# Kernel optimization log

Hardware: AMD Instinct MI355X
Metric: run time of the kernel (lower is better)

The kernel has to match this reference:

```python
import jax, jax.numpy as jnp
import numpy as np

DROPOUT_P = 0.1  # module-level constant in the source
DROP_KEY = jax.random.key(42)

B, H, S, D = 4, 16, 1024, 64


def setup_inputs() -> dict:
    key = jax.random.key(0)
    kq, kk, kv = jax.random.split(key, 3)
    return {
        "query": jax.random.normal(kq, (B, H, S, D), dtype=jnp.float32),
        "key": jax.random.normal(kk, (B, H, S, D), dtype=jnp.float32),
        "value": jax.random.normal(kv, (B, H, S, D), dtype=jnp.float32),
        "scale_factor": 8,
    }


def reference(query, key, value, scale_factor):
    # qk = query @ key^T                         [B,H,S,S]
    qk = jnp.einsum("bhqd,bhkd->bhqk", query, key)
    # source divides by inv_scale = 1/scale_factor -> multiply by scale_factor
    scaled_qk = qk * jnp.float32(scale_factor)
    softmax_qk = jax.nn.softmax(scaled_qk, axis=-1)
    # inverted dropout with fixed key (deterministic reference)
    keep = jax.random.bernoulli(DROP_KEY, 1.0 - DROPOUT_P, softmax_qk.shape)
    dropout_qk = jnp.where(keep, softmax_qk / (1.0 - DROPOUT_P), 0.0)
    # output = attn @ value                      [B,H,S,D]
    return jnp.einsum("bhqk,bhkd->bhqd", dropout_qk, value)
```

## Files before the change

### kernel.cpp

```cpp
#include <hip/hip_runtime.h>
#include <stdint.h>
#include <math.h>


constexpr int Bn = 4, Hn = 16, Sn = 1024, Dn = 64;
constexpr int NT = 256;
constexpr int TQ = 128, TK = 64;
constexpr int PST = 72;
constexpr int CAP = 512;

typedef short s16x8 __attribute__((ext_vector_type(8)));
typedef float f32x4 __attribute__((ext_vector_type(4)));

__device__ __forceinline__ uint16_t f2bf(float x) {
  uint32_t u = __float_as_uint(x);
  return (uint16_t)((u + 0x7fffu + ((u >> 16) & 1u)) >> 16);
}
__device__ __forceinline__ float bf2f(uint16_t h) {
  return __uint_as_float(((uint32_t)h) << 16);
}

__device__ __forceinline__ void tf_round(uint32_t& x0, uint32_t& x1, const int r) {
  x0 += x1;
  x1 = (x1 << r) | (x1 >> (32 - r));
  x1 ^= x0;
}

__device__ __noinline__ int keep_bit(uint32_t j) {
  uint32_t x0 = 0u, x1 = j;
  const uint32_t k0 = 0u, k1v = 42u;
  const uint32_t k2v = k0 ^ k1v ^ 0x1BD11BDAu;
  x0 += k0; x1 += k1v;
  tf_round(x0, x1, 13); tf_round(x0, x1, 15); tf_round(x0, x1, 26); tf_round(x0, x1, 6);
  x0 += k1v; x1 += k2v + 1u;
  tf_round(x0, x1, 17); tf_round(x0, x1, 29); tf_round(x0, x1, 16); tf_round(x0, x1, 24);
  x0 += k2v; x1 += k0 + 2u;
  tf_round(x0, x1, 13); tf_round(x0, x1, 15); tf_round(x0, x1, 26); tf_round(x0, x1, 6);
  x0 += k0; x1 += k1v + 3u;
  tf_round(x0, x1, 17); tf_round(x0, x1, 29); tf_round(x0, x1, 16); tf_round(x0, x1, 24);
  x0 += k1v; x1 += k2v + 4u;
  tf_round(x0, x1, 13); tf_round(x0, x1, 15); tf_round(x0, x1, 26); tf_round(x0, x1, 6);
  x0 += k2v; x1 += k0 + 5u;
  uint32_t bits = x0 ^ x1;
  float u = __uint_as_float((bits >> 9) | 0x3f800000u) - 1.0f;
  return u < 0.9f;
}

__global__ __launch_bounds__(NT) void prep_kv(const float* __restrict__ K,
                                              const float* __restrict__ V,
                                              uint16_t* __restrict__ Khg,
                                              uint16_t* __restrict__ Klg,
                                              uint16_t* __restrict__ Vtg) {
  __shared__ float Vl[TK][Dn + 1];
  const int t = threadIdx.x;
  const int kt = blockIdx.x;
  const int bh = blockIdx.y;
  const int r = t >> 2, qd = t & 3;
  const size_t tile = ((size_t)bh * 16 + kt) * 4096;
  const float* ksrc = K + ((size_t)bh * Sn + (size_t)(kt * TK + r)) * Dn + qd * 16;
  const float* vsrc = V + ((size_t)bh * Sn + (size_t)(kt * TK + r)) * Dn + qd * 16;

#pragma unroll
  for (int half = 0; half < 2; ++half) {
    float4 a = *(const float4*)(ksrc + half * 8);
    float4 b = *(const float4*)(ksrc + half * 8 + 4);
    float xs[8] = {a.x, a.y, a.z, a.w, b.x, b.y, b.z, b.w};
    s16x8 hv, lv;
#pragma unroll
    for (int j = 0; j < 8; ++j) {
      uint16_t hb = f2bf(xs[j]);
      hv[j] = (short)hb;
      lv[j] = (short)f2bf(xs[j] - bf2f(hb));
    }
    const int sc = (qd * 2 + half) ^ (r & 7);
    *(s16x8*)&Khg[tile + (size_t)r * 64 + sc * 8] = hv;
    *(s16x8*)&Klg[tile + (size_t)r * 64 + sc * 8] = lv;
    float4 va = *(const float4*)(vsrc + half * 8);
    float4 vb = *(const float4*)(vsrc + half * 8 + 4);
    *(float4*)&Vl[r][qd * 16 + half * 8] = va;
    *(float4*)&Vl[r][qd * 16 + half * 8 + 4] = vb;
  }
  __syncthreads();
#pragma unroll
  for (int half = 0; half < 2; ++half) {
    s16x8 ov;
#pragma unroll
    for (int j = 0; j < 8; ++j) ov[j] = (short)f2bf(Vl[qd * 16 + half * 8 + j][r]);
    const int sc = (qd * 2 + half) ^ (r & 7);
    *(s16x8*)&Vtg[tile + (size_t)r * 64 + sc * 8] = ov;
  }
}

__global__ __launch_bounds__(NT) void attn_mfma3(
    const float* __restrict__ Q, const uint16_t* __restrict__ Khg,
    const uint16_t* __restrict__ Klg, const uint16_t* __restrict__ Vtg,
    const float* __restrict__ V, const int* __restrict__ scale_ptr,
    float* __restrict__ out) {
  __shared__ uint16_t KhS[TK * Dn];
  __shared__ uint16_t KlS[TK * Dn];
  __shared__ uint16_t VtS[Dn * TK];
  __shared__ uint16_t PS[4 * 32 * PST];
  __shared__ uint32_t Lm[4][CAP];
  __shared__ float Lsv[4][CAP];
  __shared__ float mfin[4][32];

  const int t = threadIdx.x;
  const int w = t >> 6;
  const int lane = t & 63;
  const int l16 = lane & 15;
  const int quad = lane >> 4;

  const int b = blockIdx.z, h = blockIdx.y;
  const int qbase = blockIdx.x * TQ;
  const int bh = b * Hn + h;
  const float qscale = (float)(*scale_ptr);

  s16x8 qh[2][2], ql[2][2];
#pragma unroll
  for (int u = 0; u < 2; ++u) {
    const int qrow = qbase + u * 64 + w * 16 + l16;
    const float* src = Q + ((size_t)bh * Sn + (size_t)qrow) * Dn;
#pragma unroll
    for (int ks = 0; ks < 2; ++ks) {
      float4 x0 = *(const float4*)(src + ks * 32 + quad * 8);
      float4 x1 = *(const float4*)(src + ks * 32 + quad * 8 + 4);
      float xv[8] = {x0.x, x0.y, x0.z, x0.w, x1.x, x1.y, x1.z, x1.w};
#pragma unroll
      for (int j = 0; j < 8; ++j) {
        const float xs = xv[j] * qscale;
        uint16_t hb = f2bf(xs);
        qh[u][ks][j] = (short)hb;
        ql[u][ks][j] = (short)f2bf(xs - bf2f(hb));
      }
    }
  }

  float m_r[2][4], l_r[2][4];
#pragma unroll
  for (int u = 0; u < 2; ++u)
#pragma unroll
    for (int r = 0; r < 4; ++r) { m_r[u][r] = -INFINITY; l_r[u][r] = 0.0f; }
  f32x4 o_acc[2][4];
#pragma unroll
  for (int u = 0; u < 2; ++u)
#pragma unroll
    for (int c = 0; c < 4; ++c) o_acc[u][c] = (f32x4){0.f, 0.f, 0.f, 0.f};

  const uint32_t hbase = (uint32_t)bh * (uint32_t)Sn;
  int lbase = 0;

  for (int kt = 0; kt < Sn / TK; ++kt) {
    const int kbase = kt * TK;
    __syncthreads();

    {
      const size_t tile = ((size_t)bh * 16 + kt) * 4096;
#pragma unroll
      for (int s = 0; s < 2; ++s) {
        const int eoff = (w * 2 + s) * 512 + lane * 8;
        __builtin_amdgcn_global_load_lds(
            (const __attribute__((address_space(1))) uint32_t*)(Khg + tile + eoff),
            (__attribute__((address_space(3))) uint32_t*)(KhS + eoff), 16, 0, 0);
        __builtin_amdgcn_global_load_lds(
            (const __attribute__((address_space(1))) uint32_t*)(Klg + tile + eoff),
            (__attribute__((address_space(3))) uint32_t*)(KlS + eoff), 16, 0, 0);
        __builtin_amdgcn_global_load_lds(
            (const __attribute__((address_space(1))) uint32_t*)(Vtg + tile + eoff),
            (__attribute__((address_space(3))) uint32_t*)(VtS + eoff), 16, 0, 0);
      }
    }
    __syncthreads();

    f32x4 sacc[2][4];
#pragma unroll
    for (int u = 0; u < 2; ++u)
#pragma unroll
      for (int c = 0; c < 4; ++c) sacc[u][c] = (f32x4){0.f, 0.f, 0.f, 0.f};
#pragma unroll
    for (int ks = 0; ks < 2; ++ks) {
#pragma unroll
      for (int c = 0; c < 4; ++c) {
        const int boff = (c * 16 + l16) * 64 + (((ks * 4 + quad) ^ (l16 & 7)) * 8);
        const s16x8 bhv = *(const s16x8*)&KhS[boff];
        const s16x8 blv = *(const s16x8*)&KlS[boff];
#pragma unroll
        for (int u = 0; u < 2; ++u) {
          sacc[u][c] = __builtin_amdgcn_mfma_f32_16x16x32_bf16(qh[u][ks], bhv, sacc[u][c], 0, 0, 0);
          sacc[u][c] = __builtin_amdgcn_mfma_f32_16x16x32_bf16(ql[u][ks], bhv, sacc[u][c], 0, 0, 0);
          sacc[u][c] = __builtin_amdgcn_mfma_f32_16x16x32_bf16(qh[u][ks], blv, sacc[u][c], 0, 0, 0);
        }
      }
    }

#pragma unroll
    for (int u = 0; u < 2; ++u) {
      float mx[4], al[4];
#pragma unroll
      for (int r = 0; r < 4; ++r) {
        mx[r] = fmaxf(fmaxf(sacc[u][0][r], sacc[u][1][r]),
                      fmaxf(sacc[u][2][r], sacc[u][3][r]));
#pragma unroll
        for (int d = 1; d < 16; d <<= 1) mx[r] = fmaxf(mx[r], __shfl_xor(mx[r], d));
        const float mn = fmaxf(m_r[u][r], mx[r]);
        al[r] = __expf(m_r[u][r] - mn);
        m_r[u][r] = mn;
      }
#pragma unroll
      for (int c = 0; c < 4; ++c)
#pragma unroll
        for (int r = 0; r < 4; ++r) o_acc[u][c][r] *= al[r];

      float rs[4] = {0.f, 0.f, 0.f, 0.f};
#pragma unroll
      for (int r = 0; r < 4; ++r) {
        float dv[4], pv[4];
#pragma unroll
        for (int c = 0; c < 4; ++c) {
          dv[c] = sacc[u][c][r] - m_r[u][r];
          pv[c] = __expf(dv[c]);
          rs[r] += pv[c];
        }
        const float dmx = fmaxf(fmaxf(dv[0], dv[1]), fmaxf(dv[2], dv[3]));
        if (__ballot(dmx > -11.0f) != 0ull) {
#pragma unroll
          for (int c = 0; c < 4; ++c) {
            const uint64_t mc = __ballot(dv[c] > -11.0f);
            if (mc != 0ull) {
              if (lbase + 64 <= CAP) {
                const int slot = lbase + (int)__popcll(mc & ((1ull << lane) - 1ull));
                if (dv[c] > -11.0f) {
                  const uint32_t rw = (uint32_t)(u * 16 + quad * 4 + r);
                  Lm[w][slot] = (rw << 10) | (uint32_t)(kbase + c * 16 + l16);
                  Lsv[w][slot] = dv[c] + m_r[u][r];
                }
                lbase += (int)__popcll(mc);
              } else if (dv[c] > -11.0f) {
                const uint32_t j =
                    (hbase + (uint32_t)(qbase + u * 64 + w * 16 + quad * 4 + r)) *
                        (uint32_t)Sn +
                    (uint32_t)(kbase + c * 16 + l16);
                if (!keep_bit(j)) pv[c] = 0.0f;
              }
            }
          }
        }
        const int prow = (w * 32 + u * 16 + quad * 4 + r) * PST;
#pragma unroll
        for (int c = 0; c < 4; ++c) PS[prow + c * 16 + l16] = f2bf(pv[c]);
      }
#pragma unroll
      for (int r = 0; r < 4; ++r) {
#pragma unroll
        for (int d = 1; d < 16; d <<= 1) rs[r] += __shfl_xor(rs[r], d);
        l_r[u][r] = l_r[u][r] * al[r] + rs[r];
      }
    }

#pragma unroll
    for (int ks2 = 0; ks2 < 2; ++ks2) {
      s16x8 pa[2];
#pragma unroll
      for (int u = 0; u < 2; ++u)
        pa[u] = *(const s16x8*)&PS[(w * 32 + u * 16 + l16) * PST + ks2 * 32 + quad * 8];
#pragma unroll
      for (int c = 0; c < 4; ++c) {
        const int voff = (c * 16 + l16) * 64 + (((ks2 * 4 + quad) ^ (l16 & 7)) * 8);
        const s16x8 vb = *(const s16x8*)&VtS[voff];
#pragma unroll
        for (int u = 0; u < 2; ++u)
          o_acc[u][c] = __builtin_amdgcn_mfma_f32_16x16x32_bf16(pa[u], vb, o_acc[u][c], 0, 0, 0);
      }
    }
  }

  if (l16 == 0) {
#pragma unroll
    for (int u = 0; u < 2; ++u)
#pragma unroll
      for (int r = 0; r < 4; ++r) mfin[w][u * 16 + quad * 4 + r] = m_r[u][r];
  }
  for (int e0 = 0; e0 < lbase; e0 += 64) {
    const int e = e0 + lane;
    const bool valid = e < lbase;
    const uint32_t meta = valid ? Lm[w][e] : 0u;
    const float sv = valid ? Lsv[w][e] : 0.0f;
    const uint32_t rwv = meta >> 10, keyv = meta & 1023u;
    const uint32_t grow = (uint32_t)qbase + (rwv >> 4) * 64u + (uint32_t)(w * 16) + (rwv & 15u);
    const uint32_t j = (hbase + grow) * (uint32_t)Sn + keyv;
    const int kb = keep_bit(j);
    uint64_t dm = __ballot(valid && !kb);
    while (dm != 0ull) {
      const int src = (int)__builtin_ctzll(dm);
      dm &= dm - 1ull;
      const uint32_t meta_s = (uint32_t)__builtin_amdgcn_readlane((int)meta, src);
      const float sv_s =
          __uint_as_float((uint32_t)__builtin_amdgcn_readlane((int)__float_as_uint(sv), src));
      const int rw = (int)(meta_s >> 10);
      const int key = (int)(meta_s & 1023u);
      const int urw = rw >> 4, rr = rw & 3, qo = (rw >> 2) & 3;
      const float p = __expf(sv_s - mfin[w][rw]);
      const float pb = bf2f(f2bf(p));
      const float* vp = V + ((size_t)bh * Sn + (size_t)key) * Dn;
#pragma unroll
      for (int u = 0; u < 2; ++u)
        if (u == urw) {
#pragma unroll
          for (int r = 0; r < 4; ++r)
            if (r == rr) {
              if (quad == qo) {
#pragma unroll
                for (int c = 0; c < 4; ++c) {
                  const float vv = bf2f(f2bf(vp[c * 16 + l16]));
                  o_acc[u][c][r] = fmaf(-pb, vv, o_acc[u][c][r]);
                }
              }
            }
        }
    }
  }

#pragma unroll
  for (int u = 0; u < 2; ++u) {
    float inv[4];
#pragma unroll
    for (int r = 0; r < 4; ++r) inv[r] = 1.0f / (l_r[u][r] * 0.9f);
#pragma unroll
    for (int c = 0; c < 4; ++c)
#pragma unroll
      for (int r = 0; r < 4; ++r)
        out[((size_t)bh * Sn + (size_t)(qbase + u * 64 + w * 16 + quad * 4 + r)) * Dn +
            c * 16 + l16] = o_acc[u][c][r] * inv[r];
  }
}

constexpr int KST = 72;
__global__ __launch_bounds__(NT) void attn_fallback(
    const float* __restrict__ Q, const float* __restrict__ K,
    const float* __restrict__ V, const int* __restrict__ scale_ptr,
    float* __restrict__ out) {
  __shared__ uint16_t KhS[64 * KST];
  __shared__ uint16_t KlS[64 * KST];
  __shared__ uint16_t VtS[Dn * KST];
  __shared__ uint16_t PSf[4 * 16 * KST];

  const int t = threadIdx.x;
  const int w = t >> 6;
  const int lane = t & 63;
  const int l16 = lane & 15;
  const int quad = lane >> 4;
  const int b = blockIdx.z, h = blockIdx.y;
  const int qbase = blockIdx.x * 64;
  const size_t bh = (size_t)b * Hn + h;
  const float scale = (float)(*scale_ptr);
  const float* Kp = K + bh * Sn * Dn;
  const float* Vp = V + bh * Sn * Dn;

  const int qrow = qbase + w * 16 + l16;
  const float* Qp = Q + (bh * Sn + (size_t)qrow) * Dn;
  s16x8 qh[2], ql[2];
#pragma unroll
  for (int ks = 0; ks < 2; ++ks) {
    const float* src = Qp + ks * 32 + quad * 8;
    float4 x0 = *(const float4*)(src);
    float4 x1 = *(const float4*)(src + 4);
    float xv[8] = {x0.x, x0.y, x0.z, x0.w, x1.x, x1.y, x1.z, x1.w};
#pragma unroll
    for (int j = 0; j < 8; ++j) {
      uint16_t hb = f2bf(xv[j]);
      qh[ks][j] = (short)hb;
      ql[ks][j] = (short)f2bf(xv[j] - bf2f(hb));
    }
  }
  const int kr = t >> 2;
  const int qd = t & 3;
  float m_r[4], l_r[4];
#pragma unroll
  for (int r = 0; r < 4; ++r) { m_r[r] = -INFINITY; l_r[r] = 0.0f; }
  f32x4 o_acc[4];
#pragma unroll
  for (int c = 0; c < 4; ++c) o_acc[c] = (f32x4){0.f, 0.f, 0.f, 0.f};
  const uint32_t rowlin = ((uint32_t)(b * Hn + h)) * (uint32_t)Sn +
                          (uint32_t)(qbase + w * 16 + quad * 4);
  for (int kt = 0; kt < Sn / 64; ++kt) {
    const int kbase = kt * 64;
    __syncthreads();
    {
      const float* ksrc = Kp + (size_t)(kbase + kr) * Dn + qd * 16;
#pragma unroll
      for (int half = 0; half < 2; ++half) {
        float4 a = *(const float4*)(ksrc + half * 8);
        float4 b2 = *(const float4*)(ksrc + half * 8 + 4);
        float xs[8] = {a.x, a.y, a.z, a.w, b2.x, b2.y, b2.z, b2.w};
        s16x8 hv, lv;
#pragma unroll
        for (int j = 0; j < 8; ++j) {
          uint16_t hb = f2bf(xs[j]);
          hv[j] = (short)hb;
          lv[j] = (short)f2bf(xs[j] - bf2f(hb));
        }
        *(s16x8*)&KhS[kr * KST + qd * 16 + half * 8] = hv;
        *(s16x8*)&KlS[kr * KST + qd * 16 + half * 8] = lv;
      }
      const float* vsrc = Vp + (size_t)(kbase + kr) * Dn + qd * 16;
#pragma unroll
      for (int half = 0; half < 2; ++half) {
        float4 a = *(const float4*)(vsrc + half * 8);
        float4 b2 = *(const float4*)(vsrc + half * 8 + 4);
        float xs[8] = {a.x, a.y, a.z, a.w, b2.x, b2.y, b2.z, b2.w};
#pragma unroll
        for (int j = 0; j < 8; ++j)
          VtS[(qd * 16 + half * 8 + j) * KST + kr] = f2bf(xs[j]);
      }
    }
    __syncthreads();
    f32x4 sacc[4];
#pragma unroll
    for (int c = 0; c < 4; ++c) sacc[c] = (f32x4){0.f, 0.f, 0.f, 0.f};
#pragma unroll
    for (int ks = 0; ks < 2; ++ks) {
#pragma unroll
      for (int c = 0; c < 4; ++c) {
        const s16x8 bh_ = *(const s16x8*)&KhS[(c * 16 + l16) * KST + ks * 32 + quad * 8];
        const s16x8 bl_ = *(const s16x8*)&KlS[(c * 16 + l16) * KST + ks * 32 + quad * 8];
        sacc[c] = __builtin_amdgcn_mfma_f32_16x16x32_bf16(qh[ks], bh_, sacc[c], 0, 0, 0);
        sacc[c] = __builtin_amdgcn_mfma_f32_16x16x32_bf16(ql[ks], bh_, sacc[c], 0, 0, 0);
        sacc[c] = __builtin_amdgcn_mfma_f32_16x16x32_bf16(qh[ks], bl_, sacc[c], 0, 0, 0);
      }
    }
    float mx[4];
#pragma unroll
    for (int r = 0; r < 4; ++r) {
      mx[r] = sacc[0][r] * scale;
#pragma unroll
      for (int c = 1; c < 4; ++c) mx[r] = fmaxf(mx[r], sacc[c][r] * scale);
#pragma unroll
      for (int d = 1; d < 16; d <<= 1) mx[r] = fmaxf(mx[r], __shfl_xor(mx[r], d));
    }
    float al[4];
#pragma unroll
    for (int r = 0; r < 4; ++r) {
      const float mn = fmaxf(m_r[r], mx[r]);
      al[r] = __expf(m_r[r] - mn);
      m_r[r] = mn;
    }
#pragma unroll
    for (int c = 0; c < 4; ++c)
#pragma unroll
      for (int r = 0; r < 4; ++r) o_acc[c][r] *= al[r];
    float rs[4] = {0.f, 0.f, 0.f, 0.f};
#pragma unroll
    for (int c = 0; c < 4; ++c) {
#pragma unroll
      for (int r = 0; r < 4; ++r) {
        const float d = sacc[c][r] * scale - m_r[r];
        float pv = __expf(d);
        rs[r] += pv;
        if (d > -25.0f) {
          const uint32_t j = (rowlin + (uint32_t)r) * (uint32_t)Sn +
                             (uint32_t)(kbase + c * 16 + l16);
          if (!keep_bit(j)) pv = 0.0f;
        }
        PSf[(w * 16 + quad * 4 + r) * KST + c * 16 + l16] = f2bf(pv);
      }
    }
#pragma unroll
    for (int r = 0; r < 4; ++r) {
#pragma unroll
      for (int d = 1; d < 16; d <<= 1) rs[r] += __shfl_xor(rs[r], d);
      l_r[r] = l_r[r] * al[r] + rs[r];
    }
#pragma unroll
    for (int ks2 = 0; ks2 < 2; ++ks2) {
      const s16x8 pa = *(const s16x8*)&PSf[(w * 16 + l16) * KST + ks2 * 32 + quad * 8];
#pragma unroll
      for (int c = 0; c < 4; ++c) {
        const s16x8 vb = *(const s16x8*)&VtS[(c * 16 + l16) * KST + ks2 * 32 + quad * 8];
        o_acc[c] = __builtin_amdgcn_mfma_f32_16x16x32_bf16(pa, vb, o_acc[c], 0, 0, 0);
      }
    }
  }
  float inv[4];
#pragma unroll
  for (int r = 0; r < 4; ++r) inv[r] = 1.0f / (l_r[r] * 0.9f);
#pragma unroll
  for (int c = 0; c < 4; ++c)
#pragma unroll
    for (int r = 0; r < 4; ++r)
      out[(bh * Sn + (size_t)(qbase + w * 16 + quad * 4 + r)) * Dn + c * 16 + l16] =
          o_acc[c][r] * inv[r];
}

extern "C" void kernel_launch(void* const* d_in, const int* in_sizes, int n_in,
                              void* d_out, int out_size, void* d_ws, size_t ws_size,
                              hipStream_t stream) {
  const float* Q = (const float*)d_in[0];
  const float* K = (const float*)d_in[1];
  const float* V = (const float*)d_in[2];
  const int* sf = (const int*)d_in[3];
  float* out = (float*)d_out;

  constexpr size_t ARR = (size_t)Bn * Hn * Sn * Dn;
  const size_t need = 3 * ARR * sizeof(uint16_t);

  if (ws_size >= need) {
    uint16_t* Khg = (uint16_t*)d_ws;
    uint16_t* Klg = Khg + ARR;
    uint16_t* Vtg = Klg + ARR;
    prep_kv<<<dim3(16, 64), NT, 0, stream>>>(K, V, Khg, Klg, Vtg);
    attn_mfma3<<<dim3(Sn / TQ, Hn, Bn), NT, 0, stream>>>(Q, Khg, Klg, Vtg, V, sf, out);
  } else {
    attn_fallback<<<dim3(Sn / 64, Hn, Bn), NT, 0, stream>>>(Q, K, V, sf, out);
  }
}
```

Measured before the change: 196.9 us.

## Double-buffer K/V tiles in LDS with async prefetch of next tile

New measurement: 198.2 us. Within noise of the previous version (+0.7%).

```diff
diff --git a/kernel.cpp b/kernel.cpp
--- a/kernel.cpp
+++ b/kernel.cpp
@@ -7,7 +7,7 @@
 constexpr int NT = 256;
 constexpr int TQ = 128, TK = 64;
 constexpr int PST = 72;
-constexpr int CAP = 512;
+constexpr int CAP = 256;
 
 typedef short s16x8 __attribute__((ext_vector_type(8)));
 typedef float f32x4 __attribute__((ext_vector_type(4)));
@@ -91,14 +91,14 @@
   }
 }
 
-__global__ __launch_bounds__(NT) void attn_mfma3(
+__global__ __launch_bounds__(NT) void attn_mfma4(
     const float* __restrict__ Q, const uint16_t* __restrict__ Khg,
     const uint16_t* __restrict__ Klg, const uint16_t* __restrict__ Vtg,
     const float* __restrict__ V, const int* __restrict__ scale_ptr,
     float* __restrict__ out) {
-  __shared__ uint16_t KhS[TK * Dn];
-  __shared__ uint16_t KlS[TK * Dn];
-  __shared__ uint16_t VtS[Dn * TK];
+  __shared__ uint16_t KhS[2][TK * Dn];
+  __shared__ uint16_t KlS[2][TK * Dn];
+  __shared__ uint16_t VtS[2][TK * Dn];
   __shared__ uint16_t PS[4 * 32 * PST];
   __shared__ uint32_t Lm[4][CAP];
   __shared__ float Lsv[4][CAP];
@@ -115,6 +115,32 @@
   const int bh = b * Hn + h;
   const float qscale = (float)(*scale_ptr);
 
+  const int e0off = (w * 2) * 512 + lane * 8;
+  const int e1off = (w * 2 + 1) * 512 + lane * 8;
+  const size_t tbase = (size_t)bh * 16 * 4096;
+
+  {
+    const size_t tile = tbase;
+    __builtin_amdgcn_global_load_lds(
+        (const __attribute__((address_space(1))) uint32_t*)(Khg + tile + e0off),
+        (__attribute__((address_space(3))) uint32_t*)(&KhS[0][0] + e0off), 16, 0, 0);
+    __builtin_amdgcn_global_load_lds(
+        (const __attribute__((address_space(1))) uint32_t*)(Khg + tile + e1off),
+        (__attribute__((address_space(3))) uint32_t*)(&KhS[0][0] + e1off), 16, 0, 0);
+    __builtin_amdgcn_global_load_lds(
+        (const __attribute__((address_space(1))) uint32_t*)(Klg + tile + e0off),
+        (__attribute__((address_space(3))) uint32_t*)(&KlS[0][0] + e0off), 16, 0, 0);
+    __builtin_amdgcn_global_load_lds(
+        (const __attribute__((address_space(1))) uint32_t*)(Klg + tile + e1off),
+        (__attribute__((address_space(3))) uint32_t*)(&KlS[0][0] + e1off), 16, 0, 0);
+    __builtin_amdgcn_global_load_lds(
+        (const __attribute__((address_space(1))) uint32_t*)(Vtg + tile + e0off),
+        (__attribute__((address_space(3))) uint32_t*)(&VtS[0][0] + e0off), 16, 0, 0);
+    __builtin_amdgcn_global_load_lds(
+        (const __attribute__((address_space(1))) uint32_t*)(Vtg + tile + e1off),
+        (__attribute__((address_space(3))) uint32_t*)(&VtS[0][0] + e1off), 16, 0, 0);
+  }
+
   s16x8 qh[2][2], ql[2][2];
 #pragma unroll
   for (int u = 0; u < 2; ++u) {
@@ -151,25 +177,31 @@
 
   for (int kt = 0; kt < Sn / TK; ++kt) {
     const int kbase = kt * TK;
+    const int cur = kt & 1;
     __syncthreads();
 
-    {
-      const size_t tile = ((size_t)bh * 16 + kt) * 4096;
-#pragma unroll
-      for (int s = 0; s < 2; ++s) {
-        const int eoff = (w * 2 + s) * 512 + lane * 8;
-        __builtin_amdgcn_global_load_lds(
-            (const __attribute__((address_space(1))) uint32_t*)(Khg + tile + eoff),
-            (__attribute__((address_space(3))) uint32_t*)(KhS + eoff), 16, 0, 0);
-        __builtin_amdgcn_global_load_lds(
-            (const __attribute__((address_space(1))) uint32_t*)(Klg + tile + eoff),
-            (__attribute__((address_space(3))) uint32_t*)(KlS + eoff), 16, 0, 0);
-        __builtin_amdgcn_global_load_lds(
-            (const __attribute__((address_space(1))) uint32_t*)(Vtg + tile + eoff),
-            (__attribute__((address_space(3))) uint32_t*)(VtS + eoff), 16, 0, 0);
-      }
-    }
-    __syncthreads();
+    if (kt + 1 < Sn / TK) {
+      const size_t tile = tbase + (size_t)(kt + 1) * 4096;
+      const int nxt = cur ^ 1;
+      __builtin_amdgcn_global_load_lds(
+          (const __attribute__((address_space(1))) uint32_t*)(Khg + tile + e0off),
+          (__attribute__((address_space(3))) uint32_t*)(&KhS[nxt][0] + e0off), 16, 0, 0);
+      __builtin_amdgcn_global_load_lds(
+          (const __attribute__((address_space(1))) uint32_t*)(Khg + tile + e1off),
+          (__attribute__((address_space(3))) uint32_t*)(&KhS[nxt][0] + e1off), 16, 0, 0);
+      __builtin_amdgcn_global_load_lds(
+          (const __attribute__((address_space(1))) uint32_t*)(Klg + tile + e0off),
+          (__attribute__((address_space(3))) uint32_t*)(&KlS[nxt][0] + e0off), 16, 0, 0);
+      __builtin_amdgcn_global_load_lds(
+          (const __attribute__((address_space(1))) uint32_t*)(Klg + tile + e1off),
+          (__attribute__((address_space(3))) uint32_t*)(&KlS[nxt][0] + e1off), 16, 0, 0);
+      __builtin_amdgcn_global_load_lds(
+          (const __attribute__((address_space(1))) uint32_t*)(Vtg + tile + e0off),
+          (__attribute__((address_space(3))) uint32_t*)(&VtS[nxt][0] + e0off), 16, 0, 0);
+      __builtin_amdgcn_global_load_lds(
+          (const __attribute__((address_space(1))) uint32_t*)(Vtg + tile + e1off),
+          (__attribute__((address_space(3))) uint32_t*)(&VtS[nxt][0] + e1off), 16, 0, 0);
+    }
 
     f32x4 sacc[2][4];
 #pragma unroll
@@ -181,8 +213,8 @@
 #pragma unroll
       for (int c = 0; c < 4; ++c) {
         const int boff = (c * 16 + l16) * 64 + (((ks * 4 + quad) ^ (l16 & 7)) * 8);
-        const s16x8 bhv = *(const s16x8*)&KhS[boff];
-        const s16x8 blv = *(const s16x8*)&KlS[boff];
+        const s16x8 bhv = *(const s16x8*)&KhS[cur][boff];
+        const s16x8 blv = *(const s16x8*)&KlS[cur][boff];
 #pragma unroll
         for (int u = 0; u < 2; ++u) {
           sacc[u][c] = __builtin_amdgcn_mfma_f32_16x16x32_bf16(qh[u][ks], bhv, sacc[u][c], 0, 0, 0);
@@ -265,7 +297,7 @@
 #pragma unroll
       for (int c = 0; c < 4; ++c) {
         const int voff = (c * 16 + l16) * 64 + (((ks2 * 4 + quad) ^ (l16 & 7)) * 8);
-        const s16x8 vb = *(const s16x8*)&VtS[voff];
+        const s16x8 vb = *(const s16x8*)&VtS[cur][voff];
 #pragma unroll
         for (int u = 0; u < 2; ++u)
           o_acc[u][c] = __builtin_amdgcn_mfma_f32_16x16x32_bf16(pa[u], vb, o_acc[u][c], 0, 0, 0);
@@ -507,7 +539,7 @@
     uint16_t* Klg = Khg + ARR;
     uint16_t* Vtg = Klg + ARR;
     prep_kv<<<dim3(16, 64), NT, 0, stream>>>(K, V, Khg, Klg, Vtg);
-    attn_mfma3<<<dim3(Sn / TQ, Hn, Bn), NT, 0, stream>>>(Q, Khg, Klg, Vtg, V, sf, out);
+    attn_mfma4<<<dim3(Sn / TQ, Hn, Bn), NT, 0, stream>>>(Q, Khg, Klg, Vtg, V, sf, out);
   } else {
     attn_fallback<<<dim3(Sn / 64, Hn, Bn), NT, 0, stream>>>(Q, K, V, sf, out);
   }
```

## Transpose MFMA operands so each lane owns one query row in attention

Applied to the files above, without the earlier changes.

Result: slower. 247.1 us (+25.5%).

```diff
diff --git a/kernel.cpp b/kernel.cpp
--- a/kernel.cpp
+++ b/kernel.cpp
@@ -6,10 +6,10 @@
 constexpr int Bn = 4, Hn = 16, Sn = 1024, Dn = 64;
 constexpr int NT = 256;
 constexpr int TQ = 128, TK = 64;
-constexpr int PST = 72;
-constexpr int CAP = 512;
+constexpr int CAP = 256;
 
 typedef short s16x8 __attribute__((ext_vector_type(8)));
+typedef short s16x4 __attribute__((ext_vector_type(4)));
 typedef float f32x4 __attribute__((ext_vector_type(4)));
 
 __device__ __forceinline__ uint16_t f2bf(float x) {
@@ -91,15 +91,15 @@
   }
 }
 
-__global__ __launch_bounds__(NT) void attn_mfma3(
+__global__ __launch_bounds__(NT) void attn_mfma5(
     const float* __restrict__ Q, const uint16_t* __restrict__ Khg,
     const uint16_t* __restrict__ Klg, const uint16_t* __restrict__ Vtg,
     const float* __restrict__ V, const int* __restrict__ scale_ptr,
     float* __restrict__ out) {
   __shared__ uint16_t KhS[TK * Dn];
   __shared__ uint16_t KlS[TK * Dn];
-  __shared__ uint16_t VtS[Dn * TK];
-  __shared__ uint16_t PS[4 * 32 * PST];
+  __shared__ uint16_t VtS[TK * Dn];
+  __shared__ uint16_t PS[4 * 32 * 64];
   __shared__ uint32_t Lm[4][CAP];
   __shared__ float Lsv[4][CAP];
   __shared__ float mfin[4][32];
@@ -109,16 +109,22 @@
   const int lane = t & 63;
   const int l16 = lane & 15;
   const int quad = lane >> 4;
+  const int xl = l16 & 7;
 
   const int b = blockIdx.z, h = blockIdx.y;
   const int qbase = blockIdx.x * TQ;
   const int bh = b * Hn + h;
   const float qscale = (float)(*scale_ptr);
 
+  const int e0off = (w * 2) * 512 + lane * 8;
+  const int e1off = (w * 2 + 1) * 512 + lane * 8;
+  const size_t tbase = (size_t)bh * 16 * 4096;
+  const int psw = w * 2048;
+
   s16x8 qh[2][2], ql[2][2];
 #pragma unroll
   for (int u = 0; u < 2; ++u) {
-    const int qrow = qbase + u * 64 + w * 16 + l16;
+    const int qrow = qbase + w * 32 + u * 16 + l16;
     const float* src = Q + ((size_t)bh * Sn + (size_t)qrow) * Dn;
 #pragma unroll
     for (int ks = 0; ks < 2; ++ks) {
@@ -135,11 +141,8 @@
     }
   }
 
-  float m_r[2][4], l_r[2][4];
-#pragma unroll
-  for (int u = 0; u < 2; ++u)
-#pragma unroll
-    for (int r = 0; r < 4; ++r) { m_r[u][r] = -INFINITY; l_r[u][r] = 0.0f; }
+  float m_r[2] = {-INFINITY, -INFINITY};
+  float l_r[2] = {0.0f, 0.0f};
   f32x4 o_acc[2][4];
 #pragma unroll
   for (int u = 0; u < 2; ++u)
@@ -154,20 +157,25 @@
     __syncthreads();
 
     {
-      const size_t tile = ((size_t)bh * 16 + kt) * 4096;
-#pragma unroll
-      for (int s = 0; s < 2; ++s) {
-        const int eoff = (w * 2 + s) * 512 + lane * 8;
-        __builtin_amdgcn_global_load_lds(
-            (const __attribute__((address_space(1))) uint32_t*)(Khg + tile + eoff),
-            (__attribute__((address_space(3))) uint32_t*)(KhS + eoff), 16, 0, 0);
-        __builtin_amdgcn_global_load_lds(
-            (const __attribute__((address_space(1))) uint32_t*)(Klg + tile + eoff),
-            (__attribute__((address_space(3))) uint32_t*)(KlS + eoff), 16, 0, 0);
-        __builtin_amdgcn_global_load_lds(
-            (const __attribute__((address_space(1))) uint32_t*)(Vtg + tile + eoff),
-            (__attribute__((address_space(3))) uint32_t*)(VtS + eoff), 16, 0, 0);
-      }
+      const size_t tile = tbase + (size_t)kt * 4096;
+      __builtin_amdgcn_global_load_lds(
+          (const __attribute__((address_space(1))) uint32_t*)(Khg + tile + e0off),
+          (__attribute__((address_space(3))) uint32_t*)(KhS + e0off), 16, 0, 0);
+      __builtin_amdgcn_global_load_lds(
+          (const __attribute__((address_space(1))) uint32_t*)(Khg + tile + e1off),
+          (__attribute__((address_space(3))) uint32_t*)(KhS + e1off), 16, 0, 0);
+      __builtin_amdgcn_global_load_lds(
+          (const __attribute__((address_space(1))) uint32_t*)(Klg + tile + e0off),
+          (__attribute__((address_space(3))) uint32_t*)(KlS + e0off), 16, 0, 0);
+      __builtin_amdgcn_global_load_lds(
+          (const __attribute__((address_space(1))) uint32_t*)(Klg + tile + e1off),
+          (__attribute__((address_space(3))) uint32_t*)(KlS + e1off), 16, 0, 0);
+      __builtin_amdgcn_global_load_lds(
+          (const __attribute__((address_space(1))) uint32_t*)(Vtg + tile + e0off),
+          (__attribute__((address_space(3))) uint32_t*)(VtS + e0off), 16, 0, 0);
+      __builtin_amdgcn_global_load_lds(
+          (const __attribute__((address_space(1))) uint32_t*)(Vtg + tile + e1off),
+          (__attribute__((address_space(3))) uint32_t*)(VtS + e1off), 16, 0, 0);
     }
     __syncthreads();
 
@@ -180,104 +188,105 @@
     for (int ks = 0; ks < 2; ++ks) {
 #pragma unroll
       for (int c = 0; c < 4; ++c) {
-        const int boff = (c * 16 + l16) * 64 + (((ks * 4 + quad) ^ (l16 & 7)) * 8);
-        const s16x8 bhv = *(const s16x8*)&KhS[boff];
-        const s16x8 blv = *(const s16x8*)&KlS[boff];
+        const int boff = (c * 16 + l16) * 64 + (((ks * 4 + quad) ^ xl) * 8);
+        const s16x8 khv = *(const s16x8*)&KhS[boff];
+        const s16x8 klv = *(const s16x8*)&KlS[boff];
 #pragma unroll
         for (int u = 0; u < 2; ++u) {
-          sacc[u][c] = __builtin_amdgcn_mfma_f32_16x16x32_bf16(qh[u][ks], bhv, sacc[u][c], 0, 0, 0);
-          sacc[u][c] = __builtin_amdgcn_mfma_f32_16x16x32_bf16(ql[u][ks], bhv, sacc[u][c], 0, 0, 0);
-          sacc[u][c] = __builtin_amdgcn_mfma_f32_16x16x32_bf16(qh[u][ks], blv, sacc[u][c], 0, 0, 0);
+          sacc[u][c] = __builtin_amdgcn_mfma_f32_16x16x32_bf16(khv, qh[u][ks], sacc[u][c], 0, 0, 0);
+          sacc[u][c] = __builtin_amdgcn_mfma_f32_16x16x32_bf16(khv, ql[u][ks], sacc[u][c], 0, 0, 0);
+          sacc[u][c] = __builtin_amdgcn_mfma_f32_16x16x32_bf16(klv, qh[u][ks], sacc[u][c], 0, 0, 0);
         }
       }
     }
 
 #pragma unroll
     for (int u = 0; u < 2; ++u) {
-      float mx[4], al[4];
-#pragma unroll
-      for (int r = 0; r < 4; ++r) {
-        mx[r] = fmaxf(fmaxf(sacc[u][0][r], sacc[u][1][r]),
-                      fmaxf(sacc[u][2][r], sacc[u][3][r]));
-#pragma unroll
-        for (int d = 1; d < 16; d <<= 1) mx[r] = fmaxf(mx[r], __shfl_xor(mx[r], d));
-        const float mn = fmaxf(m_r[u][r], mx[r]);
-        al[r] = __expf(m_r[u][r] - mn);
-        m_r[u][r] = mn;
-      }
+      float mx = sacc[u][0][0];
 #pragma unroll
       for (int c = 0; c < 4; ++c)
 #pragma unroll
-        for (int r = 0; r < 4; ++r) o_acc[u][c][r] *= al[r];
-
-      float rs[4] = {0.f, 0.f, 0.f, 0.f};
-#pragma unroll
-      for (int r = 0; r < 4; ++r) {
-        float dv[4], pv[4];
-#pragma unroll
-        for (int c = 0; c < 4; ++c) {
-          dv[c] = sacc[u][c][r] - m_r[u][r];
-          pv[c] = __expf(dv[c]);
-          rs[r] += pv[c];
+        for (int r = 0; r < 4; ++r) mx = fmaxf(mx, sacc[u][c][r]);
+      mx = fmaxf(mx, __shfl_xor(mx, 16));
+      mx = fmaxf(mx, __shfl_xor(mx, 32));
+      const float mn = fmaxf(m_r[u], mx);
+      const float al = __expf(m_r[u] - mn);
+      m_r[u] = mn;
+#pragma unroll
+      for (int c = 0; c < 4; ++c)
+#pragma unroll
+        for (int r = 0; r < 4; ++r) o_acc[u][c][r] *= al;
+
+      float pv[4][4], dvv[4][4];
+      float rs = 0.0f;
+#pragma unroll
+      for (int c = 0; c < 4; ++c)
+#pragma unroll
+        for (int r = 0; r < 4; ++r) {
+          dvv[c][r] = sacc[u][c][r] - mn;
+          pv[c][r] = __expf(dvv[c][r]);
+          rs += pv[c][r];
         }
-        const float dmx = fmaxf(fmaxf(dv[0], dv[1]), fmaxf(dv[2], dv[3]));
-        if (__ballot(dmx > -11.0f) != 0ull) {
-#pragma unroll
-          for (int c = 0; c < 4; ++c) {
-            const uint64_t mc = __ballot(dv[c] > -11.0f);
+
+      if (__ballot(mx - mn > -11.0f) != 0ull) {
+#pragma unroll
+        for (int c = 0; c < 4; ++c)
+#pragma unroll
+          for (int r = 0; r < 4; ++r) {
+            const uint64_t mc = __ballot(dvv[c][r] > -11.0f);
             if (mc != 0ull) {
               if (lbase + 64 <= CAP) {
                 const int slot = lbase + (int)__popcll(mc & ((1ull << lane) - 1ull));
-                if (dv[c] > -11.0f) {
-                  const uint32_t rw = (uint32_t)(u * 16 + quad * 4 + r);
-                  Lm[w][slot] = (rw << 10) | (uint32_t)(kbase + c * 16 + l16);
-                  Lsv[w][slot] = dv[c] + m_r[u][r];
+                if (dvv[c][r] > -11.0f) {
+                  const uint32_t rw = (uint32_t)(u * 16 + l16);
+                  Lm[w][slot] = (rw << 10) | (uint32_t)(kbase + c * 16 + quad * 4 + r);
+                  Lsv[w][slot] = dvv[c][r] + mn;
                 }
                 lbase += (int)__popcll(mc);
-              } else if (dv[c] > -11.0f) {
+              } else if (dvv[c][r] > -11.0f) {
                 const uint32_t j =
-                    (hbase + (uint32_t)(qbase + u * 64 + w * 16 + quad * 4 + r)) *
-                        (uint32_t)Sn +
-                    (uint32_t)(kbase + c * 16 + l16);
-                if (!keep_bit(j)) pv[c] = 0.0f;
+                    (hbase + (uint32_t)(qbase + w * 32 + u * 16 + l16)) * (uint32_t)Sn +
+                    (uint32_t)(kbase + c * 16 + quad * 4 + r);
+                if (!keep_bit(j)) pv[c][r] = 0.0f;
               }
             }
           }
-        }
-        const int prow = (w * 32 + u * 16 + quad * 4 + r) * PST;
-#pragma unroll
-        for (int c = 0; c < 4; ++c) PS[prow + c * 16 + l16] = f2bf(pv[c]);
-      }
-#pragma unroll
-      for (int r = 0; r < 4; ++r) {
-#pragma unroll
-        for (int d = 1; d < 16; d <<= 1) rs[r] += __shfl_xor(rs[r], d);
-        l_r[u][r] = l_r[u][r] * al[r] + rs[r];
-      }
+      }
+
+#pragma unroll
+      for (int c = 0; c < 4; ++c) {
+        s16x4 pk;
+#pragma unroll
+        for (int r = 0; r < 4; ++r) pk[r] = (short)f2bf(pv[c][r]);
+        const int pos = (c * 2 + (quad >> 1)) ^ xl;
+        *(s16x4*)&PS[psw + (u * 16 + l16) * 64 + pos * 8 + (quad & 1) * 4] = pk;
+      }
+
+      rs += __shfl_xor(rs, 16);
+      rs += __shfl_xor(rs, 32);
+      l_r[u] = l_r[u] * al + rs;
     }
 
 #pragma unroll
     for (int ks2 = 0; ks2 < 2; ++ks2) {
-      s16x8 pa[2];
+      s16x8 pb[2];
 #pragma unroll
       for (int u = 0; u < 2; ++u)
-        pa[u] = *(const s16x8*)&PS[(w * 32 + u * 16 + l16) * PST + ks2 * 32 + quad * 8];
+        pb[u] = *(const s16x8*)&PS[psw + (u * 16 + l16) * 64 + (((ks2 * 4 + quad) ^ xl) * 8)];
 #pragma unroll
       for (int c = 0; c < 4; ++c) {
-        const int voff = (c * 16 + l16) * 64 + (((ks2 * 4 + quad) ^ (l16 & 7)) * 8);
+        const int voff = (c * 16 + l16) * 64 + (((ks2 * 4 + quad) ^ xl) * 8);
         const s16x8 vb = *(const s16x8*)&VtS[voff];
 #pragma unroll
         for (int u = 0; u < 2; ++u)
-          o_acc[u][c] = __builtin_amdgcn_mfma_f32_16x16x32_bf16(pa[u], vb, o_acc[u][c], 0, 0, 0);
-      }
-    }
-  }
-
-  if (l16 == 0) {
-#pragma unroll
-    for (int u = 0; u < 2; ++u)
-#pragma unroll
-      for (int r = 0; r < 4; ++r) mfin[w][u * 16 + quad * 4 + r] = m_r[u][r];
+          o_acc[u][c] = __builtin_amdgcn_mfma_f32_16x16x32_bf16(vb, pb[u], o_acc[u][c], 0, 0, 0);
+      }
+    }
+  }
+
+  if (quad == 0) {
+#pragma unroll
+    for (int u = 0; u < 2; ++u) mfin[w][u * 16 + l16] = m_r[u];
   }
   for (int e0 = 0; e0 < lbase; e0 += 64) {
     const int e = e0 + lane;
@@ -285,7 +294,7 @@
     const uint32_t meta = valid ? Lm[w][e] : 0u;
     const float sv = valid ? Lsv[w][e] : 0.0f;
     const uint32_t rwv = meta >> 10, keyv = meta & 1023u;
-    const uint32_t grow = (uint32_t)qbase + (rwv >> 4) * 64u + (uint32_t)(w * 16) + (rwv & 15u);
+    const uint32_t grow = (uint32_t)(qbase + w * 32) + rwv;
     const uint32_t j = (hbase + grow) * (uint32_t)Sn + keyv;
     const int kb = keep_bit(j);
     uint64_t dm = __ballot(valid && !kb);
@@ -297,39 +306,46 @@
           __uint_as_float((uint32_t)__builtin_amdgcn_readlane((int)__float_as_uint(sv), src));
       const int rw = (int)(meta_s >> 10);
       const int key = (int)(meta_s & 1023u);
-      const int urw = rw >> 4, rr = rw & 3, qo = (rw >> 2) & 3;
       const float p = __expf(sv_s - mfin[w][rw]);
-      const float pb = bf2f(f2bf(p));
-      const float* vp = V + ((size_t)bh * Sn + (size_t)key) * Dn;
-#pragma unroll
-      for (int u = 0; u < 2; ++u)
-        if (u == urw) {
-#pragma unroll
-          for (int r = 0; r < 4; ++r)
-            if (r == rr) {
-              if (quad == qo) {
-#pragma unroll
-                for (int c = 0; c < 4; ++c) {
-                  const float vv = bf2f(f2bf(vp[c * 16 + l16]));
-                  o_acc[u][c][r] = fmaf(-pb, vv, o_acc[u][c][r]);
-                }
-              }
-            }
+      const float pb2 = bf2f(f2bf(p));
+      if ((rw & 15) == l16) {
+        const float* vp = V + ((size_t)bh * Sn + (size_t)key) * Dn;
+        if ((rw >> 4) == 0) {
+#pragma unroll
+          for (int c = 0; c < 4; ++c) {
+            float4 vv = *(const float4*)(vp + c * 16 + quad * 4);
+            o_acc[0][c][0] = fmaf(-pb2, bf2f(f2bf(vv.x)), o_acc[0][c][0]);
+            o_acc[0][c][1] = fmaf(-pb2, bf2f(f2bf(vv.y)), o_acc[0][c][1]);
+            o_acc[0][c][2] = fmaf(-pb2, bf2f(f2bf(vv.z)), o_acc[0][c][2]);
+            o_acc[0][c][3] = fmaf(-pb2, bf2f(f2bf(vv.w)), o_acc[0][c][3]);
+          }
+        } else {
+#pragma unroll
+          for (int c = 0; c < 4; ++c) {
+            float4 vv = *(const float4*)(vp + c * 16 + quad * 4);
+            o_acc[1][c][0] = fmaf(-pb2, bf2f(f2bf(vv.x)), o_acc[1][c][0]);
+            o_acc[1][c][1] = fmaf(-pb2, bf2f(f2bf(vv.y)), o_acc[1][c][1]);
+            o_acc[1][c][2] = fmaf(-pb2, bf2f(f2bf(vv.z)), o_acc[1][c][2]);
+            o_acc[1][c][3] = fmaf(-pb2, bf2f(f2bf(vv.w)), o_acc[1][c][3]);
+          }
         }
+      }
     }
   }
 
 #pragma unroll
   for (int u = 0; u < 2; ++u) {
-    float inv[4];
-#pragma unroll
-    for (int r = 0; r < 4; ++r) inv[r] = 1.0f / (l_r[u][r] * 0.9f);
-#pragma unroll
-    for (int c = 0; c < 4; ++c)
-#pragma unroll
-      for (int r = 0; r < 4; ++r)
-        out[((size_t)bh * Sn + (size_t)(qbase + u * 64 + w * 16 + quad * 4 + r)) * Dn +
-            c * 16 + l16] = o_acc[u][c][r] * inv[r];
+    const float inv = 1.0f / (l_r[u] * 0.9f);
+    const size_t obase = ((size_t)bh * Sn + (size_t)(qbase + w * 32 + u * 16 + l16)) * Dn;
+#pragma unroll
+    for (int c = 0; c < 4; ++c) {
+      float4 ov;
+      ov.x = o_acc[u][c][0] * inv;
+      ov.y = o_acc[u][c][1] * inv;
+      ov.z = o_acc[u][c][2] * inv;
+      ov.w = o_acc[u][c][3] * inv;
+      *(float4*)(out + obase + c * 16 + quad * 4) = ov;
+    }
   }
 }
 
@@ -507,7 +523,7 @@
     uint16_t* Klg = Khg + ARR;
     uint16_t* Vtg = Klg + ARR;
     prep_kv<<<dim3(16, 64), NT, 0, stream>>>(K, V, Khg, Klg, Vtg);
-    attn_mfma3<<<dim3(Sn / TQ, Hn, Bn), NT, 0, stream>>>(Q, Khg, Klg, Vtg, V, sf, out);
+    attn_mfma5<<<dim3(Sn / TQ, Hn, Bn), NT, 0, stream>>>(Q, Khg, Klg, Vtg, V, sf, out);
   } else {
     attn_fallback<<<dim3(Sn / 64, Hn, Bn), NT, 0, stream>>>(Q, K, V, sf, out);
   }
```
